# Optimization experiments

Hardware: AMD Instinct MI355X
Metric: run time of the kernel (lower is better)

Reference implementation:

```python
import jax, jax.numpy as jnp
import numpy as np

L, B, D, H = 512, 128, 512, 1024  # length, batch, input_dim, hidden


def setup_inputs() -> dict:
    key = jax.random.key(0)
    ks = jax.random.split(key, 5)
    s_in = 1.0 / np.sqrt(D + H)
    return {
        "x": jax.random.normal(ks[0], (L, B, D), dtype=jnp.float32),
        "h0": jax.random.normal(ks[1], (B, H), dtype=jnp.float32),
        "W_z": jax.random.normal(ks[2], (H, D + H), dtype=jnp.float32) * s_in,
        "b_z": jnp.zeros((H,), dtype=jnp.float32),
        "W_r": jax.random.normal(ks[3], (H, D + H), dtype=jnp.float32) * s_in,
        "b_r": jnp.zeros((H,), dtype=jnp.float32),
        "W_h": jax.random.normal(ks[4], (H, D + H), dtype=jnp.float32) * s_in,
        "b_h": jnp.zeros((H,), dtype=jnp.float32),
    }


def reference(x, h0, W_z, b_z, W_r, b_r, W_h, b_h):
    # GRU recurrence: gates computed from concat([h, x]) as in the torch code.
    def step(h, x_t):
        hx = jnp.concatenate([h, x_t], axis=-1)            # [B, H+D]
        z = jax.nn.sigmoid(hx @ W_z.T + b_z)               # update gate
        r = jax.nn.sigmoid(hx @ W_r.T + b_r)               # reset gate
        rhx = jnp.concatenate([r * h, x_t], axis=-1)       # [B, H+D]
        h_tilde = jnp.tanh(rhx @ W_h.T + b_h)
        h_new = (1.0 - z) * h + z * h_tilde
        return h_new, h_new

    _, outputs = jax.lax.scan(step, h0, x)  # outputs: [L, B, H]
    return outputs
```

## Files before the change

kernel.cpp:

```cpp
#include <hip/hip_runtime.h>
#include <cstdint>
#include <cstddef>

#define LT 512
#define BB 128
#define DD 512
#define HH 1024
#define HD 1536
#define MT (LT*BB)

typedef __bf16 bf16;
typedef __bf16 bf16x8 __attribute__((ext_vector_type(8)));
typedef __bf16 bf16x4 __attribute__((ext_vector_type(4)));
typedef float  f32x4  __attribute__((ext_vector_type(4)));

#define O_WZR 0u
#define O_WHR 6291456u
#define O_WXH 8388608u
#define O_XB  9437184u
#define O_HB  76546048u
#define O_RHB 76808192u
#define O_BAR 77594624u
#define O_FLG 77660160u
#define WS_NEED 77922304u

#define WAIT_VM0() asm volatile("s_waitcnt vmcnt(0)" ::: "memory")
#define SCHED0()   __builtin_amdgcn_sched_barrier(0)
#define L1_INV()   asm volatile("buffer_inv sc0" ::: "memory")

template<int L> __device__ __forceinline__ f32x4 ld16s(const void* p) {
  f32x4 r;
  if constexpr (L) asm volatile("global_load_dwordx4 %0, %1, off sc0"     : "=&v"(r) : "v"(p) : "memory");
  else             asm volatile("global_load_dwordx4 %0, %1, off sc0 sc1" : "=&v"(r) : "v"(p) : "memory");
  return r;
}
template<int L> __device__ __forceinline__ unsigned ld2s(const void* p) {
  unsigned r;
  if constexpr (L) asm volatile("global_load_ushort %0, %1, off sc0"     : "=&v"(r) : "v"(p) : "memory");
  else             asm volatile("global_load_ushort %0, %1, off sc0 sc1" : "=&v"(r) : "v"(p) : "memory");
  return r;
}
template<int L> __device__ __forceinline__ void st2s(bf16* p, unsigned v) {
  if constexpr (L) asm volatile("global_store_short %0, %1, off sc0"     :: "v"(p), "v"(v) : "memory");
  else             asm volatile("global_store_short %0, %1, off sc0 sc1" :: "v"(p), "v"(v) : "memory");
}
__device__ __forceinline__ void st_flag(unsigned char* p, unsigned v) {
  asm volatile("global_store_byte %0, %1, off sc0" :: "v"(p), "v"(v) : "memory");
}
__device__ __forceinline__ unsigned ld_flag(const unsigned char* p) {
  unsigned r;
  asm volatile("global_load_ubyte %0, %1, off sc0\n\ts_waitcnt vmcnt(0)"
               : "=&v"(r) : "v"(p) : "memory");
  return r;
}
__device__ __forceinline__ unsigned bf16_bits(float f) {
  bf16 b = (bf16)f;
  return (unsigned)__builtin_bit_cast(unsigned short, b);
}
__device__ __forceinline__ float bits_to_f32(unsigned u16) {
  return __builtin_bit_cast(float, u16 << 16);
}

__device__ __forceinline__ void bar_sync(unsigned* cntA, unsigned char* flagst,
                                         int t, int voteok, int& use_local,
                                         unsigned tgtA, int tid, int lane, int wv, int sb) {
  WAIT_VM0();
  __syncthreads();
  if (tid == 0)
    __hip_atomic_fetch_add(cntA, 1u, __ATOMIC_RELAXED, __HIP_MEMORY_SCOPE_AGENT);
  if (wv == 0) {
    if (tid == 0 && voteok) st_flag(flagst + sb, 1u);
    int done = 0;
    if (use_local && t >= 2) {
      int gd = 1500;
      while (gd--) {
        L1_INV();
        unsigned ok = 1u;
        if (lane < 32) ok = ld_flag(flagst + lane);
        if (__ballot(ok != 0u) == ~0ull) { done = 1; break; }
      }
      if (!done) use_local = 0;
    }
    if (!done && tid == 0) {
      int gd = 60000;
      while (__hip_atomic_load(cntA, __ATOMIC_RELAXED, __HIP_MEMORY_SCOPE_AGENT) < tgtA
             && --gd) __builtin_amdgcn_s_sleep(2);
    }
    L1_INV();
  }
  __syncthreads();
}

__global__ void k_cvt(const float* __restrict__ s, bf16* __restrict__ d, int n8) {
  int i = blockIdx.x*256 + threadIdx.x;
  if (i >= n8) return;
  const float4* p = (const float4*)s + (size_t)i*2;
  float4 a = p[0], b = p[1];
  bf16x8 v = {(bf16)a.x,(bf16)a.y,(bf16)a.z,(bf16)a.w,(bf16)b.x,(bf16)b.y,(bf16)b.z,(bf16)b.w};
  *((bf16x8*)d + i) = v;
}

__global__ void k_split_wh(const float* __restrict__ Wh, bf16* __restrict__ whr, bf16* __restrict__ wxh) {
  int i = blockIdx.x*256 + threadIdx.x;
  if (i >= 1024*192) return;
  int row = i / 192, c8 = (i % 192)*8;
  const float4* p = (const float4*)(Wh + (size_t)row*HD + c8);
  float4 a = p[0], b = p[1];
  bf16x8 v = {(bf16)a.x,(bf16)a.y,(bf16)a.z,(bf16)a.w,(bf16)b.x,(bf16)b.y,(bf16)b.z,(bf16)b.w};
  bf16* dptr = (c8 < HH) ? (whr + (size_t)row*HH + c8) : (wxh + (size_t)row*DD + (c8 - HH));
  *(bf16x8*)dptr = v;
}

__global__ void k_init_h(const float* __restrict__ h0, bf16* __restrict__ hb) {
  int i = blockIdx.x*256 + threadIdx.x;
  float4 a = ((const float4*)h0)[i];
  bf16x4 v = {(bf16)a.x,(bf16)a.y,(bf16)a.z,(bf16)a.w};
  *((bf16x4*)hb + i) = v;
}

__global__ __launch_bounds__(256) void k_gemm_xh(
    const bf16* __restrict__ xb, const bf16* __restrict__ wxh,
    const float* __restrict__ bh, float* __restrict__ out)
{
  __shared__ char As[16384];
  __shared__ char Bs[16384];
  const int bid = blockIdx.x;
  const int nt8 = bid & 7, mtb = bid >> 3;
  const int tid = threadIdx.x;
  const int lane = tid & 63, wv = tid >> 6;
  const int l15 = lane & 15, q = lane >> 4;
  const int wm = wv >> 1, wn = wv & 1;
  f32x4 acc[4][4] = {};
  const char* Ab = (const char*)(xb + (size_t)mtb*128*DD);
  const char* Bb = (const char*)(wxh + (size_t)nt8*128*DD);
  const int crow = tid >> 3, ccb = (tid & 7)*16;
  const int cdst = crow*128 + (ccb ^ ((crow & 7) << 4));
  for (int kt = 0; kt < 8; ++kt) {
    __syncthreads();
    #pragma unroll
    for (int i = 0; i < 4; ++i) {
      *(uint4*)(As + cdst + i*4096) = *(const uint4*)(Ab + (size_t)(crow + i*32)*1024 + kt*128 + ccb);
      *(uint4*)(Bs + cdst + i*4096) = *(const uint4*)(Bb + (size_t)(crow + i*32)*1024 + kt*128 + ccb);
    }
    __syncthreads();
    #pragma unroll
    for (int ks = 0; ks < 2; ++ks) {
      bf16x8 af[4], bfr[4];
      #pragma unroll
      for (int m4 = 0; m4 < 4; ++m4) {
        int row = wm*64 + m4*16 + l15, cb = ks*64 + 16*q;
        af[m4] = *(const bf16x8*)(As + row*128 + (cb ^ ((row&7)<<4)));
      }
      #pragma unroll
      for (int n4 = 0; n4 < 4; ++n4) {
        int row = wn*64 + n4*16 + l15, cb = ks*64 + 16*q;
        bfr[n4] = *(const bf16x8*)(Bs + row*128 + (cb ^ ((row&7)<<4)));
      }
      #pragma unroll
      for (int m4 = 0; m4 < 4; ++m4)
        #pragma unroll
        for (int n4 = 0; n4 < 4; ++n4)
          acc[m4][n4] = __builtin_amdgcn_mfma_f32_16x16x32_bf16(af[m4], bfr[n4], acc[m4][n4], 0, 0, 0);
    }
  }
  const int jb = nt8*128 + wn*64;
  const size_t mb = (size_t)mtb*128 + wm*64;
  #pragma unroll
  for (int n4 = 0; n4 < 4; ++n4) {
    int j = jb + n4*16 + l15;
    float bias = bh[j];
    #pragma unroll
    for (int m4 = 0; m4 < 4; ++m4)
      #pragma unroll
      for (int e = 0; e < 4; ++e) {
        size_t m = mb + m4*16 + 4*q + e;
        out[m*HH + j] = acc[m4][n4][e] + bias;
      }
  }
}

struct Frags { bf16x8 zr[4][2]; bf16x8 h[8]; };

template<int L>
__device__ __forceinline__ void tloop(const Frags& F, char* ldsW, char* scr, float* zsL,
    const bf16* __restrict__ xb, float* __restrict__ out,
    bf16* __restrict__ hb, bf16* __restrict__ rhb,
    unsigned* cnt1A, unsigned* cnt2A, unsigned char* flg1, unsigned char* flg2,
    int voteok, int g, int sb, int ch, int kh, int tid, int lane, int wv,
    const float (&bias)[2], float (&hreg)[4])
{
  const int l15 = lane & 15, q = lane >> 4;
  const bf16* hrow = hb  + (size_t)(g*16 + l15)*HH;
  const bf16* rrow = rhb + (size_t)(g*16 + l15)*HH;
  const int kh384 = kh*384, kh256 = kh*256;
  const int jown = sb*32 + ch*16 + l15;
  int use_local = L ? voteok : 0;

  for (int t = 0; t < LT; ++t) {
    {
      f32x4 ab[12];
      const bf16* xrow = xb + (size_t)(t*BB + g*16 + l15)*DD;
      #pragma unroll
      for (int kk = 0; kk < 12; ++kk) {
        int kabs = kh384 + kk*32;
        if (kabs < HH) ab[kk] = ld16s<L>(hrow + kabs + 8*q);
        else           ab[kk] = *(const f32x4*)(xrow + (kabs - HH) + 8*q);
      }
      unsigned hv[2][4];
      if (ch == 1 && kh == 0) {
        #pragma unroll
        for (int nt = 0; nt < 2; ++nt) {
          int cr = sb*32 + nt*16 + l15;
          #pragma unroll
          for (int e = 0; e < 4; ++e)
            hv[nt][e] = ld2s<L>(hb + (size_t)(g*16 + 4*q + e)*HH + cr);
        }
      }
      WAIT_VM0(); SCHED0();
      f32x4 a0 = {}, a1 = {};
      #pragma unroll
      for (int kk = 0; kk < 12; ++kk) {
        bf16x8 a = __builtin_bit_cast(bf16x8, ab[kk]);
        bf16x8 b0, b1;
        if (kk < 8) {
          b0 = *(const bf16x8*)(ldsW + (ch*32      + l15)*2064 + kh*512 + kk*64 + 16*q);
          b1 = *(const bf16x8*)(ldsW + (ch*32 + 16 + l15)*2064 + kh*512 + kk*64 + 16*q);
        } else { b0 = F.zr[kk-8][0]; b1 = F.zr[kk-8][1]; }
        a0 = __builtin_amdgcn_mfma_f32_16x16x32_bf16(a, b0, a0, 0, 0, 0);
        a1 = __builtin_amdgcn_mfma_f32_16x16x32_bf16(a, b1, a1, 0, 0, 0);
      }
      if (kh) {
        int s = ((kh-1)*2 + ch)*2;
        *(f32x4*)(scr + (s+0)*1024 + lane*16) = a0;
        *(f32x4*)(scr + (s+1)*1024 + lane*16) = a1;
      }
      __syncthreads();
      if (kh == 0) {
        #pragma unroll
        for (int k2 = 0; k2 < 3; ++k2) {
          int s = (k2*2 + ch)*2;
          a0 += *(const f32x4*)(scr + (s+0)*1024 + lane*16);
          a1 += *(const f32x4*)(scr + (s+1)*1024 + lane*16);
        }
        if (ch == 0) {
          #pragma unroll
          for (int nt = 0; nt < 2; ++nt) {
            f32x4 ac = nt ? a1 : a0;
            #pragma unroll
            for (int e = 0; e < 4; ++e)
              zsL[(nt*16 + l15)*16 + 4*q + e] =
                1.f/(1.f + __expf(-(ac[e] + bias[nt])));
          }
        } else {
          #pragma unroll
          for (int nt = 0; nt < 2; ++nt) {
            f32x4 ac = nt ? a1 : a0;
            int cr = sb*32 + nt*16 + l15;
            #pragma unroll
            for (int e = 0; e < 4; ++e) {
              int m = g*16 + 4*q + e;
              float gate = 1.f/(1.f + __expf(-(ac[e] + bias[nt])));
              st2s<L>(rhb + (size_t)m*HH + cr, bf16_bits(gate * bits_to_f32(hv[nt][e])));
            }
          }
        }
      }
    }
    bar_sync(cnt1A, flg1 + t*32, t, L ? voteok : 0, use_local,
             32u*(unsigned)(t+1), tid, lane, wv, sb);
    {
      f32x4 rb[8];
      #pragma unroll
      for (int kk = 0; kk < 8; ++kk)
        rb[kk] = ld16s<L>(rrow + kh256 + kk*32 + 8*q);
      float xh[4];
      if (kh == 0) {
        #pragma unroll
        for (int e = 0; e < 4; ++e)
          xh[e] = out[(size_t)t*(BB*HH) + (size_t)(g*16 + 4*q + e)*HH + jown];
      }
      WAIT_VM0(); SCHED0();
      f32x4 acc = {};
      #pragma unroll
      for (int kk = 0; kk < 8; ++kk)
        acc = __builtin_amdgcn_mfma_f32_16x16x32_bf16(
            __builtin_bit_cast(bf16x8, rb[kk]), F.h[kk], acc, 0, 0, 0);
      if (kh) *(f32x4*)(scr + ((kh-1)*2 + ch)*1024 + lane*16) = acc;
      __syncthreads();
      if (kh == 0) {
        #pragma unroll
        for (int k2 = 0; k2 < 3; ++k2)
          acc += *(const f32x4*)(scr + (k2*2 + ch)*1024 + lane*16);
        f32x4 zv = *(const f32x4*)(zsL + (ch*16 + l15)*16 + 4*q);
        #pragma unroll
        for (int e = 0; e < 4; ++e) {
          int m = g*16 + 4*q + e;
          size_t idx = (size_t)m*HH + jown;
          size_t oidx = (size_t)t*(BB*HH) + idx;
          float ht = tanhf(acc[e] + xh[e]);
          float hn = hreg[e] + zv[e]*(ht - hreg[e]);
          out[oidx] = hn;
          hreg[e] = hn;
          st2s<L>(hb + idx, bf16_bits(hn));
        }
      }
    }
    bar_sync(cnt2A, flg2 + t*32, t, L ? voteok : 0, use_local,
             32u*(unsigned)(t+1), tid, lane, wv, sb);
    if (L && tid == 0 && voteok && t + 2 < LT) {
      st_flag(flg1 + (t+2)*32 + sb, 0u);
      st_flag(flg2 + (t+2)*32 + sb, 0u);
    }
  }
}

__global__ __launch_bounds__(512) void k_gru(
    const bf16* __restrict__ Wzr, const bf16* __restrict__ Whr,
    const bf16* __restrict__ xb, const float* __restrict__ h0,
    const float* __restrict__ bz, const float* __restrict__ br,
    float* __restrict__ out,
    bf16* __restrict__ hb, bf16* __restrict__ rhb,
    unsigned* __restrict__ bar, unsigned char* __restrict__ flg)
{
  extern __shared__ char smem[];
  char*  ldsW = smem;
  char*  scr  = smem + 132096;
  float* zsL  = (float*)(smem + 144384);
  volatile int* modep = (volatile int*)(smem + 146432);

  const int tid = threadIdx.x, bid = blockIdx.x;
  const int lane = tid & 63, wv = tid >> 6;
  const int l15 = lane & 15, q = lane >> 4;
  const int g = bid & 7, sb = bid >> 3;
  const int ch = wv & 1, kh = wv >> 1;
  unsigned* grp   = bar + (size_t)g*2048;
  unsigned* cnt1A = grp + 40;
  unsigned* cnt2A = grp + 48;
  unsigned char* flg1 = flg + (size_t)g*32768;
  unsigned char* flg2 = flg + (size_t)g*32768 + 16384;

  #pragma unroll
  for (int i = 0; i < 16; ++i) {
    int ci = tid + i*512;
    int row = ci >> 7, c = ci & 127;
    int le = c*8, khs = le >> 8, rem = le & 255;
    int gr = (row < 32) ? sb*32 + row : HH + sb*32 + (row - 32);
    *(uint4*)(ldsW + row*2064 + c*16) =
      *(const uint4*)(Wzr + (size_t)gr*HD + khs*384 + rem);
  }
  Frags F;
  #pragma unroll
  for (int i = 0; i < 4; ++i)
    #pragma unroll
    for (int nt = 0; nt < 2; ++nt)
      F.zr[i][nt] = *(const bf16x8*)(Wzr
          + (size_t)((ch ? HH : 0) + sb*32 + nt*16 + l15)*HD
          + kh*384 + (8+i)*32 + 8*q);
  #pragma unroll
  for (int kk = 0; kk < 8; ++kk)
    F.h[kk] = *(const bf16x8*)(Whr + (size_t)(sb*32 + ch*16 + l15)*HH + kh*256 + kk*32 + 8*q);

  float bias[2];
  #pragma unroll
  for (int nt = 0; nt < 2; ++nt) {
    int c = sb*32 + nt*16 + l15;
    bias[nt] = (ch == 0) ? bz[c] : br[c];
  }
  float hreg[4];
  const int jown = sb*32 + ch*16 + l15;
  #pragma unroll
  for (int e = 0; e < 4; ++e)
    hreg[e] = h0[(size_t)(g*16 + 4*q + e)*HH + jown];

  if (tid == 0) {
    int xcc;
    asm("s_getreg_b32 %0, hwreg(HW_REG_XCC_ID)" : "=s"(xcc));
    __hip_atomic_store(&grp[sb], (unsigned)(xcc + 1), __ATOMIC_RELAXED, __HIP_MEMORY_SCOPE_AGENT);
    unsigned first = 0; int ok = 1;
    long budget = 200000;
    for (int i = 0; i < 32; ++i) {
      unsigned v = 0;
      while (budget > 0) {
        v = __hip_atomic_load(&grp[i], __ATOMIC_RELAXED, __HIP_MEMORY_SCOPE_AGENT);
        if (v) break;
        --budget; __builtin_amdgcn_s_sleep(8);
      }
      if (!v) { ok = 0; break; }
      if (i == 0) first = v;
      else if (v != first) { ok = 0; break; }
    }
    *modep = ok;
  }
  __syncthreads();
  int voteok = *modep;

  if (voteok) tloop<1>(F, ldsW, scr, zsL, xb, out, hb, rhb, cnt1A, cnt2A,
                       flg1, flg2, 1, g, sb, ch, kh, tid, lane, wv, bias, hreg);
  else        tloop<0>(F, ldsW, scr, zsL, xb, out, hb, rhb, cnt1A, cnt2A,
                       flg1, flg2, 0, g, sb, ch, kh, tid, lane, wv, bias, hreg);
}

extern "C" void kernel_launch(void* const* d_in, const int* in_sizes, int n_in,
                              void* d_out, int out_size, void* d_ws, size_t ws_size,
                              hipStream_t stream) {
  const float* x  = (const float*)d_in[0];
  const float* h0 = (const float*)d_in[1];
  const float* Wz = (const float*)d_in[2];
  const float* bz = (const float*)d_in[3];
  const float* Wr = (const float*)d_in[4];
  const float* br = (const float*)d_in[5];
  const float* Wh = (const float*)d_in[6];
  const float* bh = (const float*)d_in[7];
  float* out = (float*)d_out;
  char* ws = (char*)d_ws;
  if (ws_size < (size_t)WS_NEED) return;

  bf16*  wzr  = (bf16*) (ws + O_WZR);
  bf16*  whr  = (bf16*) (ws + O_WHR);
  bf16*  wxh  = (bf16*) (ws + O_WXH);
  bf16*  xbb  = (bf16*) (ws + O_XB);
  bf16*  hb   = (bf16*) (ws + O_HB);
  bf16*  rhb  = (bf16*) (ws + O_RHB);
  unsigned* bar = (unsigned*)(ws + O_BAR);
  unsigned char* flg = (unsigned char*)(ws + O_FLG);

  hipMemsetAsync(bar, 0, 65536, stream);
  k_cvt<<<16384, 256, 0, stream>>>(x, xbb, MT*DD/8);
  k_cvt<<<768, 256, 0, stream>>>(Wz, wzr, HH*HD/8);
  k_cvt<<<768, 256, 0, stream>>>(Wr, wzr + (size_t)HH*HD, HH*HD/8);
  k_split_wh<<<768, 256, 0, stream>>>(Wh, whr, wxh);
  k_init_h<<<128, 256, 0, stream>>>(h0, hb);
  k_gemm_xh<<<4096, 256, 0, stream>>>(xbb, wxh, bh, out);

  hipFuncSetAttribute((const void*)k_gru, hipFuncAttributeMaxDynamicSharedMemorySize, 146448);
  k_gru<<<256, 512, 146448, stream>>>(wzr, whr, xbb, h0, bz, br, out, hb, rhb, bar, flg);
}
```

Measured before the change: 4.616 ms.

## Prefetch next-step x and xh loads across grid barriers with partial waitcnts

Moves the loads of the next timestep's x slices into the second phase so they overlap the candidate-state MFMA and barrier, and loads the xh input term before the first barrier instead of after it. Barrier waits become partial vmcnt waits per wave role, so outstanding prefetches do not stall the grid sync. Flag resets move to a different wave earlier in the step. This shortens the serial critical path per timestep, but the hand-tuned vmcnt counts are fragile and would break silently if the number of loads per role changes.

```diff
diff --git a/kernel.cpp b/kernel.cpp
--- a/kernel.cpp
+++ b/kernel.cpp
@@ -24,9 +24,11 @@
 #define O_FLG 77660160u
 #define WS_NEED 77922304u
 
-#define WAIT_VM0() asm volatile("s_waitcnt vmcnt(0)" ::: "memory")
-#define SCHED0()   __builtin_amdgcn_sched_barrier(0)
-#define L1_INV()   asm volatile("buffer_inv sc0" ::: "memory")
+#define WAIT_VM0()  asm volatile("s_waitcnt vmcnt(0)" ::: "memory")
+#define WAIT_VM4()  asm volatile("s_waitcnt vmcnt(4)" ::: "memory")
+#define WAIT_VM12() asm volatile("s_waitcnt vmcnt(12)" ::: "memory")
+#define SCHED0()    __builtin_amdgcn_sched_barrier(0)
+#define L1_INV()    asm volatile("buffer_inv sc0" ::: "memory")
 
 template<int L> __device__ __forceinline__ f32x4 ld16s(const void* p) {
   f32x4 r;
@@ -44,6 +46,16 @@
   if constexpr (L) asm volatile("global_store_short %0, %1, off sc0"     :: "v"(p), "v"(v) : "memory");
   else             asm volatile("global_store_short %0, %1, off sc0 sc1" :: "v"(p), "v"(v) : "memory");
 }
+__device__ __forceinline__ f32x4 ld16p(const void* p) {
+  f32x4 r;
+  asm volatile("global_load_dwordx4 %0, %1, off" : "=&v"(r) : "v"(p) : "memory");
+  return r;
+}
+__device__ __forceinline__ float ld4p(const void* p) {
+  float r;
+  asm volatile("global_load_dword %0, %1, off" : "=&v"(r) : "v"(p) : "memory");
+  return r;
+}
 __device__ __forceinline__ void st_flag(unsigned char* p, unsigned v) {
   asm volatile("global_store_byte %0, %1, off sc0" :: "v"(p), "v"(v) : "memory");
 }
@@ -63,8 +75,10 @@
 
 __device__ __forceinline__ void bar_sync(unsigned* cntA, unsigned char* flagst,
                                          int t, int voteok, int& use_local,
-                                         unsigned tgtA, int tid, int lane, int wv, int sb) {
-  WAIT_VM0();
+                                         unsigned tgtA, int tid, int lane, int wv,
+                                         int sb, int ewait) {
+  if (ewait == 0)      { WAIT_VM0(); }
+  else if (ewait == 4) { WAIT_VM4(); }
   __syncthreads();
   if (tid == 0)
     __hip_atomic_fetch_add(cntA, 1u, __ATOMIC_RELAXED, __HIP_MEMORY_SCOPE_AGENT);
@@ -195,16 +209,26 @@
   const int kh384 = kh*384, kh256 = kh*256;
   const int jown = sb*32 + ch*16 + l15;
   int use_local = L ? voteok : 0;
+  const int ew1 = (kh == 0 && ch == 1) ? 4 : -1;
+  const int ew2 = (kh == 0) ? 0 : -1;
+
+  f32x4 ab[12];
+  {
+    const bf16* xrow0 = xb + (size_t)(g*16 + l15)*DD;
+    #pragma unroll
+    for (int kk = 0; kk < 12; ++kk) {
+      int kabs = kh384 + kk*32;
+      if (kabs >= HH) ab[kk] = ld16p(xrow0 + (kabs - HH) + 8*q);
+    }
+  }
 
   for (int t = 0; t < LT; ++t) {
+    float xh[4];
     {
-      f32x4 ab[12];
-      const bf16* xrow = xb + (size_t)(t*BB + g*16 + l15)*DD;
       #pragma unroll
       for (int kk = 0; kk < 12; ++kk) {
         int kabs = kh384 + kk*32;
         if (kabs < HH) ab[kk] = ld16s<L>(hrow + kabs + 8*q);
-        else           ab[kk] = *(const f32x4*)(xrow + (kabs - HH) + 8*q);
       }
       unsigned hv[2][4];
       if (ch == 1 && kh == 0) {
@@ -265,21 +289,36 @@
           }
         }
       }
+      if (L && voteok && wv == 1 && lane == 0 && t + 2 < LT) {
+        st_flag(flg1 + (t+2)*32 + sb, 0u);
+        st_flag(flg2 + (t+2)*32 + sb, 0u);
+      }
+      if (kh == 0) {
+        #pragma unroll
+        for (int e = 0; e < 4; ++e)
+          xh[e] = ld4p(out + (size_t)t*(BB*HH) + (size_t)(g*16 + 4*q + e)*HH + jown);
+      }
     }
     bar_sync(cnt1A, flg1 + t*32, t, L ? voteok : 0, use_local,
-             32u*(unsigned)(t+1), tid, lane, wv, sb);
+             32u*(unsigned)(t+1), tid, lane, wv, sb, ew1);
     {
       f32x4 rb[8];
       #pragma unroll
       for (int kk = 0; kk < 8; ++kk)
         rb[kk] = ld16s<L>(rrow + kh256 + kk*32 + 8*q);
-      float xh[4];
-      if (kh == 0) {
-        #pragma unroll
-        for (int e = 0; e < 4; ++e)
-          xh[e] = out[(size_t)t*(BB*HH) + (size_t)(g*16 + 4*q + e)*HH + jown];
-      }
-      WAIT_VM0(); SCHED0();
+      {
+        int tn = (t+1 < LT) ? t+1 : t;
+        const bf16* xrow_n = xb + (size_t)(tn*BB + g*16 + l15)*DD;
+        #pragma unroll
+        for (int kk = 0; kk < 12; ++kk) {
+          int kabs = kh384 + kk*32;
+          if (kabs >= HH) ab[kk] = ld16p(xrow_n + (kabs - HH) + 8*q);
+        }
+      }
+      if      (kh == 3) { WAIT_VM12(); }
+      else if (kh == 2) { WAIT_VM4(); }
+      else              { WAIT_VM0(); }
+      SCHED0();
       f32x4 acc = {};
       #pragma unroll
       for (int kk = 0; kk < 8; ++kk)
@@ -306,11 +345,7 @@
       }
     }
     bar_sync(cnt2A, flg2 + t*32, t, L ? voteok : 0, use_local,
-             32u*(unsigned)(t+1), tid, lane, wv, sb);
-    if (L && tid == 0 && voteok && t + 2 < LT) {
-      st_flag(flg1 + (t+2)*32 + sb, 0u);
-      st_flag(flg2 + (t+2)*32 + sb, 0u);
-    }
+             32u*(unsigned)(t+1), tid, lane, wv, sb, ew2);
   }
 }
 
```

Measured after the change: 5.095 ms. 1.1x slower.

## Split batch group into two halves and interleave phases to hide barrier latency

Applied to the files above, without the earlier changes.

Each block's 16 batch rows are split into two 8-row halves, A and B. The recurrence is software-pipelined so one half's gate phase runs while the other half's grid barrier is pending, and the barrier is split into separate arrive and wait steps. The h values needed for r*h now come from an LDS copy instead of per-element global loads. The MFMA tiles now carry 8 rows duplicated, so half of each MFMA is wasted work, and four barrier counters and flag sets replace two.

```diff
diff --git a/kernel.cpp b/kernel.cpp
--- a/kernel.cpp
+++ b/kernel.cpp
@@ -22,7 +22,7 @@
 #define O_RHB 76808192u
 #define O_BAR 77594624u
 #define O_FLG 77660160u
-#define WS_NEED 77922304u
+#define WS_NEED 78184448u
 
 #define WAIT_VM0() asm volatile("s_waitcnt vmcnt(0)" ::: "memory")
 #define SCHED0()   __builtin_amdgcn_sched_barrier(0)
@@ -34,12 +34,6 @@
   else             asm volatile("global_load_dwordx4 %0, %1, off sc0 sc1" : "=&v"(r) : "v"(p) : "memory");
   return r;
 }
-template<int L> __device__ __forceinline__ unsigned ld2s(const void* p) {
-  unsigned r;
-  if constexpr (L) asm volatile("global_load_ushort %0, %1, off sc0"     : "=&v"(r) : "v"(p) : "memory");
-  else             asm volatile("global_load_ushort %0, %1, off sc0 sc1" : "=&v"(r) : "v"(p) : "memory");
-  return r;
-}
 template<int L> __device__ __forceinline__ void st2s(bf16* p, unsigned v) {
   if constexpr (L) asm volatile("global_store_short %0, %1, off sc0"     :: "v"(p), "v"(v) : "memory");
   else             asm volatile("global_store_short %0, %1, off sc0 sc1" :: "v"(p), "v"(v) : "memory");
@@ -57,19 +51,20 @@
   bf16 b = (bf16)f;
   return (unsigned)__builtin_bit_cast(unsigned short, b);
 }
-__device__ __forceinline__ float bits_to_f32(unsigned u16) {
-  return __builtin_bit_cast(float, u16 << 16);
-}
-
-__device__ __forceinline__ void bar_sync(unsigned* cntA, unsigned char* flagst,
-                                         int t, int voteok, int& use_local,
-                                         unsigned tgtA, int tid, int lane, int wv, int sb) {
+
+__device__ __forceinline__ void bar_arrive(unsigned* cntA, unsigned char* flagst,
+                                           int voteok, int tid, int sb) {
   WAIT_VM0();
   __syncthreads();
-  if (tid == 0)
+  if (tid == 0) {
     __hip_atomic_fetch_add(cntA, 1u, __ATOMIC_RELAXED, __HIP_MEMORY_SCOPE_AGENT);
+    if (voteok) st_flag(flagst + sb, 1u);
+  }
+}
+__device__ __forceinline__ void bar_wait(unsigned* cntA, unsigned char* flagst,
+                                         int t, int& use_local, unsigned tgtA,
+                                         int lane, int wv) {
   if (wv == 0) {
-    if (tid == 0 && voteok) st_flag(flagst + sb, 1u);
     int done = 0;
     if (use_local && t >= 2) {
       int gd = 1500;
@@ -81,7 +76,7 @@
       }
       if (!done) use_local = 0;
     }
-    if (!done && tid == 0) {
+    if (!done && lane == 0) {
       int gd = 60000;
       while (__hip_atomic_load(cntA, __ATOMIC_RELAXED, __HIP_MEMORY_SCOPE_AGENT) < tgtA
              && --gd) __builtin_amdgcn_s_sleep(2);
@@ -182,134 +177,167 @@
 struct Frags { bf16x8 zr[4][2]; bf16x8 h[8]; };
 
 template<int L>
-__device__ __forceinline__ void tloop(const Frags& F, char* ldsW, char* scr, float* zsL,
+__device__ __forceinline__ void phase1(const Frags& F, char* ldsW, char* scr,
+    float* zsL_s, const bf16* hsL_s,
+    const bf16* hrow, const bf16* xrow, bf16* rhb,
+    int rb_, int sb, int ch, int kh, int lane, const float (&bias)[2])
+{
+  const int l15 = lane & 15, q = lane >> 4;
+  const int kh384 = kh*384;
+  f32x4 ab[12];
+  #pragma unroll
+  for (int kk = 0; kk < 12; ++kk) {
+    int kabs = kh384 + kk*32;
+    if (kabs < HH) ab[kk] = ld16s<L>(hrow + kabs + 8*q);
+    else           ab[kk] = *(const f32x4*)(xrow + (kabs - HH) + 8*q);
+  }
+  WAIT_VM0(); SCHED0();
+  f32x4 a0 = {}, a1 = {};
+  #pragma unroll
+  for (int kk = 0; kk < 12; ++kk) {
+    bf16x8 a = __builtin_bit_cast(bf16x8, ab[kk]);
+    bf16x8 b0, b1;
+    if (kk < 8) {
+      b0 = *(const bf16x8*)(ldsW + (ch*32      + l15)*2064 + kh*512 + kk*64 + 16*q);
+      b1 = *(const bf16x8*)(ldsW + (ch*32 + 16 + l15)*2064 + kh*512 + kk*64 + 16*q);
+    } else { b0 = F.zr[kk-8][0]; b1 = F.zr[kk-8][1]; }
+    a0 = __builtin_amdgcn_mfma_f32_16x16x32_bf16(a, b0, a0, 0, 0, 0);
+    a1 = __builtin_amdgcn_mfma_f32_16x16x32_bf16(a, b1, a1, 0, 0, 0);
+  }
+  if (kh) {
+    int s = ((kh-1)*2 + ch)*2;
+    *(f32x4*)(scr + (s+0)*1024 + lane*16) = a0;
+    *(f32x4*)(scr + (s+1)*1024 + lane*16) = a1;
+  }
+  __syncthreads();
+  if (kh == 0) {
+    #pragma unroll
+    for (int k2 = 0; k2 < 3; ++k2) {
+      int s = (k2*2 + ch)*2;
+      a0 += *(const f32x4*)(scr + (s+0)*1024 + lane*16);
+      a1 += *(const f32x4*)(scr + (s+1)*1024 + lane*16);
+    }
+    if (q < 2) {
+      int r = 4*q;
+      if (ch == 0) {
+        #pragma unroll
+        for (int nt = 0; nt < 2; ++nt) {
+          f32x4 ac = nt ? a1 : a0;
+          #pragma unroll
+          for (int e = 0; e < 4; ++e)
+            zsL_s[(nt*16 + l15)*8 + r + e] = 1.f/(1.f + __expf(-(ac[e] + bias[nt])));
+        }
+      } else {
+        #pragma unroll
+        for (int nt = 0; nt < 2; ++nt) {
+          f32x4 ac = nt ? a1 : a0;
+          int cr = sb*32 + nt*16 + l15;
+          #pragma unroll
+          for (int e = 0; e < 4; ++e) {
+            float hvf = (float)hsL_s[(nt*16 + l15)*8 + r + e];
+            float gate = 1.f/(1.f + __expf(-(ac[e] + bias[nt])));
+            st2s<L>(rhb + (size_t)(rb_ + r + e)*HH + cr, bf16_bits(gate * hvf));
+          }
+        }
+      }
+    }
+  }
+}
+
+template<int L>
+__device__ __forceinline__ void phase2(const Frags& F, char* scr,
+    const float* zsL_s, bf16* hsL_s,
+    const bf16* rrow, float* out, size_t outbase, bf16* hb,
+    int rb_, int ch, int kh, int lane, float (&hreg)[4], int jown)
+{
+  const int l15 = lane & 15, q = lane >> 4;
+  const int kh256 = kh*256;
+  f32x4 rb[8];
+  #pragma unroll
+  for (int kk = 0; kk < 8; ++kk)
+    rb[kk] = ld16s<L>(rrow + kh256 + kk*32 + 8*q);
+  float xh[4];
+  if (kh == 0 && q < 2) {
+    #pragma unroll
+    for (int e = 0; e < 4; ++e)
+      xh[e] = out[outbase + (size_t)(rb_ + 4*q + e)*HH + jown];
+  }
+  WAIT_VM0(); SCHED0();
+  f32x4 acc = {};
+  #pragma unroll
+  for (int kk = 0; kk < 8; ++kk)
+    acc = __builtin_amdgcn_mfma_f32_16x16x32_bf16(
+        __builtin_bit_cast(bf16x8, rb[kk]), F.h[kk], acc, 0, 0, 0);
+  if (kh) *(f32x4*)(scr + ((kh-1)*2 + ch)*1024 + lane*16) = acc;
+  __syncthreads();
+  if (kh == 0) {
+    #pragma unroll
+    for (int k2 = 0; k2 < 3; ++k2)
+      acc += *(const f32x4*)(scr + (k2*2 + ch)*1024 + lane*16);
+    if (q < 2) {
+      int r = 4*q;
+      #pragma unroll
+      for (int e = 0; e < 4; ++e) {
+        int m = rb_ + r + e;
+        float zv = zsL_s[(ch*16 + l15)*8 + r + e];
+        float ht = tanhf(acc[e] + xh[e]);
+        float hn = hreg[e] + zv*(ht - hreg[e]);
+        out[outbase + (size_t)m*HH + jown] = hn;
+        hreg[e] = hn;
+        unsigned hbits = bf16_bits(hn);
+        st2s<L>(hb + (size_t)m*HH + jown, hbits);
+        hsL_s[(ch*16 + l15)*8 + r + e] = __builtin_bit_cast(bf16, (unsigned short)hbits);
+      }
+    }
+  }
+}
+
+template<int L>
+__device__ __forceinline__ void tloop(const Frags& F, char* ldsW, char* scr,
+    float* zsL, bf16* hsL,
     const bf16* __restrict__ xb, float* __restrict__ out,
     bf16* __restrict__ hb, bf16* __restrict__ rhb,
-    unsigned* cnt1A, unsigned* cnt2A, unsigned char* flg1, unsigned char* flg2,
+    unsigned* cA1, unsigned* cB1, unsigned* cA2, unsigned* cB2,
+    unsigned char* fA1, unsigned char* fB1, unsigned char* fA2, unsigned char* fB2,
     int voteok, int g, int sb, int ch, int kh, int tid, int lane, int wv,
-    const float (&bias)[2], float (&hreg)[4])
+    const float (&bias)[2], float (&hregA)[4], float (&hregB)[4])
 {
-  const int l15 = lane & 15, q = lane >> 4;
-  const bf16* hrow = hb  + (size_t)(g*16 + l15)*HH;
-  const bf16* rrow = rhb + (size_t)(g*16 + l15)*HH;
-  const int kh384 = kh*384, kh256 = kh*256;
+  const int l15 = lane & 15;
+  const int rbA = g*16, rbB = g*16 + 8;
+  const bf16* hrowA = hb  + (size_t)(rbA + (l15 & 7))*HH;
+  const bf16* hrowB = hb  + (size_t)(rbB + (l15 & 7))*HH;
+  const bf16* rrowA = rhb + (size_t)(rbA + (l15 & 7))*HH;
+  const bf16* rrowB = rhb + (size_t)(rbB + (l15 & 7))*HH;
+  float* zsA = zsL;        float* zsB = zsL + 256;
+  bf16*  hsA = hsL;        bf16*  hsB = hsL + 256;
   const int jown = sb*32 + ch*16 + l15;
   int use_local = L ? voteok : 0;
 
   for (int t = 0; t < LT; ++t) {
-    {
-      f32x4 ab[12];
-      const bf16* xrow = xb + (size_t)(t*BB + g*16 + l15)*DD;
-      #pragma unroll
-      for (int kk = 0; kk < 12; ++kk) {
-        int kabs = kh384 + kk*32;
-        if (kabs < HH) ab[kk] = ld16s<L>(hrow + kabs + 8*q);
-        else           ab[kk] = *(const f32x4*)(xrow + (kabs - HH) + 8*q);
-      }
-      unsigned hv[2][4];
-      if (ch == 1 && kh == 0) {
-        #pragma unroll
-        for (int nt = 0; nt < 2; ++nt) {
-          int cr = sb*32 + nt*16 + l15;
-          #pragma unroll
-          for (int e = 0; e < 4; ++e)
-            hv[nt][e] = ld2s<L>(hb + (size_t)(g*16 + 4*q + e)*HH + cr);
-        }
-      }
-      WAIT_VM0(); SCHED0();
-      f32x4 a0 = {}, a1 = {};
-      #pragma unroll
-      for (int kk = 0; kk < 12; ++kk) {
-        bf16x8 a = __builtin_bit_cast(bf16x8, ab[kk]);
-        bf16x8 b0, b1;
-        if (kk < 8) {
-          b0 = *(const bf16x8*)(ldsW + (ch*32      + l15)*2064 + kh*512 + kk*64 + 16*q);
-          b1 = *(const bf16x8*)(ldsW + (ch*32 + 16 + l15)*2064 + kh*512 + kk*64 + 16*q);
-        } else { b0 = F.zr[kk-8][0]; b1 = F.zr[kk-8][1]; }
-        a0 = __builtin_amdgcn_mfma_f32_16x16x32_bf16(a, b0, a0, 0, 0, 0);
-        a1 = __builtin_amdgcn_mfma_f32_16x16x32_bf16(a, b1, a1, 0, 0, 0);
-      }
-      if (kh) {
-        int s = ((kh-1)*2 + ch)*2;
-        *(f32x4*)(scr + (s+0)*1024 + lane*16) = a0;
-        *(f32x4*)(scr + (s+1)*1024 + lane*16) = a1;
-      }
-      __syncthreads();
-      if (kh == 0) {
-        #pragma unroll
-        for (int k2 = 0; k2 < 3; ++k2) {
-          int s = (k2*2 + ch)*2;
-          a0 += *(const f32x4*)(scr + (s+0)*1024 + lane*16);
-          a1 += *(const f32x4*)(scr + (s+1)*1024 + lane*16);
-        }
-        if (ch == 0) {
-          #pragma unroll
-          for (int nt = 0; nt < 2; ++nt) {
-            f32x4 ac = nt ? a1 : a0;
-            #pragma unroll
-            for (int e = 0; e < 4; ++e)
-              zsL[(nt*16 + l15)*16 + 4*q + e] =
-                1.f/(1.f + __expf(-(ac[e] + bias[nt])));
-          }
-        } else {
-          #pragma unroll
-          for (int nt = 0; nt < 2; ++nt) {
-            f32x4 ac = nt ? a1 : a0;
-            int cr = sb*32 + nt*16 + l15;
-            #pragma unroll
-            for (int e = 0; e < 4; ++e) {
-              int m = g*16 + 4*q + e;
-              float gate = 1.f/(1.f + __expf(-(ac[e] + bias[nt])));
-              st2s<L>(rhb + (size_t)m*HH + cr, bf16_bits(gate * bits_to_f32(hv[nt][e])));
-            }
-          }
-        }
-      }
-    }
-    bar_sync(cnt1A, flg1 + t*32, t, L ? voteok : 0, use_local,
-             32u*(unsigned)(t+1), tid, lane, wv, sb);
-    {
-      f32x4 rb[8];
-      #pragma unroll
-      for (int kk = 0; kk < 8; ++kk)
-        rb[kk] = ld16s<L>(rrow + kh256 + kk*32 + 8*q);
-      float xh[4];
-      if (kh == 0) {
-        #pragma unroll
-        for (int e = 0; e < 4; ++e)
-          xh[e] = out[(size_t)t*(BB*HH) + (size_t)(g*16 + 4*q + e)*HH + jown];
-      }
-      WAIT_VM0(); SCHED0();
-      f32x4 acc = {};
-      #pragma unroll
-      for (int kk = 0; kk < 8; ++kk)
-        acc = __builtin_amdgcn_mfma_f32_16x16x32_bf16(
-            __builtin_bit_cast(bf16x8, rb[kk]), F.h[kk], acc, 0, 0, 0);
-      if (kh) *(f32x4*)(scr + ((kh-1)*2 + ch)*1024 + lane*16) = acc;
-      __syncthreads();
-      if (kh == 0) {
-        #pragma unroll
-        for (int k2 = 0; k2 < 3; ++k2)
-          acc += *(const f32x4*)(scr + (k2*2 + ch)*1024 + lane*16);
-        f32x4 zv = *(const f32x4*)(zsL + (ch*16 + l15)*16 + 4*q);
-        #pragma unroll
-        for (int e = 0; e < 4; ++e) {
-          int m = g*16 + 4*q + e;
-          size_t idx = (size_t)m*HH + jown;
-          size_t oidx = (size_t)t*(BB*HH) + idx;
-          float ht = tanhf(acc[e] + xh[e]);
-          float hn = hreg[e] + zv[e]*(ht - hreg[e]);
-          out[oidx] = hn;
-          hreg[e] = hn;
-          st2s<L>(hb + idx, bf16_bits(hn));
-        }
-      }
-    }
-    bar_sync(cnt2A, flg2 + t*32, t, L ? voteok : 0, use_local,
-             32u*(unsigned)(t+1), tid, lane, wv, sb);
-    if (L && tid == 0 && voteok && t + 2 < LT) {
-      st_flag(flg1 + (t+2)*32 + sb, 0u);
-      st_flag(flg2 + (t+2)*32 + sb, 0u);
+    const bf16* xrowA = xb + (size_t)(t*BB + rbA + (l15 & 7))*DD;
+    const bf16* xrowB = xb + (size_t)(t*BB + rbB + (l15 & 7))*DD;
+    const size_t outbase = (size_t)t*(BB*HH);
+    phase1<L>(F, ldsW, scr, zsA, hsA, hrowA, xrowA, rhb, rbA, sb, ch, kh, lane, bias);
+    bar_arrive(cA1, fA1 + t*32, L ? voteok : 0, tid, sb);
+    if (t > 0) {
+      bar_wait(cB2, fB2 + (t-1)*32, t-1, use_local, 32u*(unsigned)t, lane, wv);
+      if (L && voteok && tid == 0 && t + 1 < LT) {
+        st_flag(fB1 + (t+1)*32 + sb, 0u);
+        st_flag(fB2 + (t+1)*32 + sb, 0u);
+      }
+    }
+    phase1<L>(F, ldsW, scr, zsB, hsB, hrowB, xrowB, rhb, rbB, sb, ch, kh, lane, bias);
+    bar_arrive(cB1, fB1 + t*32, L ? voteok : 0, tid, sb);
+    bar_wait(cA1, fA1 + t*32, t, use_local, 32u*(unsigned)(t+1), lane, wv);
+    phase2<L>(F, scr, zsA, hsA, rrowA, out, outbase, hb, rbA, ch, kh, lane, hregA, jown);
+    bar_arrive(cA2, fA2 + t*32, L ? voteok : 0, tid, sb);
+    bar_wait(cB1, fB1 + t*32, t, use_local, 32u*(unsigned)(t+1), lane, wv);
+    phase2<L>(F, scr, zsB, hsB, rrowB, out, outbase, hb, rbB, ch, kh, lane, hregB, jown);
+    bar_arrive(cB2, fB2 + t*32, L ? voteok : 0, tid, sb);
+    bar_wait(cA2, fA2 + t*32, t, use_local, 32u*(unsigned)(t+1), lane, wv);
+    if (L && voteok && tid == 0 && t + 2 < LT) {
+      st_flag(fA1 + (t+2)*32 + sb, 0u);
+      st_flag(fA2 + (t+2)*32 + sb, 0u);
     }
   }
 }
@@ -326,18 +354,19 @@
   char*  ldsW = smem;
   char*  scr  = smem + 132096;
   float* zsL  = (float*)(smem + 144384);
-  volatile int* modep = (volatile int*)(smem + 146432);
+  bf16*  hsL  = (bf16*) (smem + 146432);
+  volatile int* modep = (volatile int*)(smem + 147456);
 
   const int tid = threadIdx.x, bid = blockIdx.x;
   const int lane = tid & 63, wv = tid >> 6;
   const int l15 = lane & 15, q = lane >> 4;
   const int g = bid & 7, sb = bid >> 3;
   const int ch = wv & 1, kh = wv >> 1;
-  unsigned* grp   = bar + (size_t)g*2048;
-  unsigned* cnt1A = grp + 40;
-  unsigned* cnt2A = grp + 48;
-  unsigned char* flg1 = flg + (size_t)g*32768;
-  unsigned char* flg2 = flg + (size_t)g*32768 + 16384;
+  unsigned* grp = bar + (size_t)g*2048;
+  unsigned* cA1 = grp + 40, *cB1 = grp + 72, *cA2 = grp + 104, *cB2 = grp + 136;
+  unsigned char* fbase = flg + (size_t)g*65536;
+  unsigned char* fA1 = fbase;          unsigned char* fB1 = fbase + 16384;
+  unsigned char* fA2 = fbase + 32768;  unsigned char* fB2 = fbase + 49152;
 
   #pragma unroll
   for (int i = 0; i < 16; ++i) {
@@ -366,11 +395,22 @@
     int c = sb*32 + nt*16 + l15;
     bias[nt] = (ch == 0) ? bz[c] : br[c];
   }
-  float hreg[4];
   const int jown = sb*32 + ch*16 + l15;
-  #pragma unroll
-  for (int e = 0; e < 4; ++e)
-    hreg[e] = h0[(size_t)(g*16 + 4*q + e)*HH + jown];
+  float hregA[4], hregB[4];
+  #pragma unroll
+  for (int e = 0; e < 4; ++e) {
+    int r = (4*q + e) & 7;
+    hregA[e] = h0[(size_t)(g*16 + r)*HH + jown];
+    hregB[e] = h0[(size_t)(g*16 + 8 + r)*HH + jown];
+  }
+  if (wv == 0 && lane < 32) {
+    int c = lane;
+    #pragma unroll
+    for (int r = 0; r < 8; ++r) {
+      hsL[c*8 + r]       = (bf16)h0[(size_t)(g*16 + r)*HH + sb*32 + c];
+      hsL[256 + c*8 + r] = (bf16)h0[(size_t)(g*16 + 8 + r)*HH + sb*32 + c];
+    }
+  }
 
   if (tid == 0) {
     int xcc;
@@ -394,10 +434,12 @@
   __syncthreads();
   int voteok = *modep;
 
-  if (voteok) tloop<1>(F, ldsW, scr, zsL, xb, out, hb, rhb, cnt1A, cnt2A,
-                       flg1, flg2, 1, g, sb, ch, kh, tid, lane, wv, bias, hreg);
-  else        tloop<0>(F, ldsW, scr, zsL, xb, out, hb, rhb, cnt1A, cnt2A,
-                       flg1, flg2, 0, g, sb, ch, kh, tid, lane, wv, bias, hreg);
+  if (voteok) tloop<1>(F, ldsW, scr, zsL, hsL, xb, out, hb, rhb,
+                       cA1, cB1, cA2, cB2, fA1, fB1, fA2, fB2,
+                       1, g, sb, ch, kh, tid, lane, wv, bias, hregA, hregB);
+  else        tloop<0>(F, ldsW, scr, zsL, hsL, xb, out, hb, rhb,
+                       cA1, cB1, cA2, cB2, fA1, fB1, fA2, fB2,
+                       0, g, sb, ch, kh, tid, lane, wv, bias, hregA, hregB);
 }
 
 extern "C" void kernel_launch(void* const* d_in, const int* in_sizes, int n_in,
@@ -432,6 +474,6 @@
   k_init_h<<<128, 256, 0, stream>>>(h0, hb);
   k_gemm_xh<<<4096, 256, 0, stream>>>(xbb, wxh, bh, out);
 
-  hipFuncSetAttribute((const void*)k_gru, hipFuncAttributeMaxDynamicSharedMemorySize, 146448);
-  k_gru<<<256, 512, 146448, stream>>>(wzr, whr, xbb, h0, bz, br, out, hb, rhb, bar, flg);
-}
+  hipFuncSetAttribute((const void*)k_gru, hipFuncAttributeMaxDynamicSharedMemorySize, 147472);
+  k_gru<<<256, 512, 147472, stream>>>(wzr, whr, xbb, h0, bz, br, out, hb, rhb, bar, flg);
+}
```

Result: slower. 10.02 ms (+117.1%).
